# Kernel optimization log

Measured on AMD Instinct MI355X. Metric: run time of the kernel, lower is better.

The kernel has to match this reference:

```python
import jax, jax.numpy as jnp
import numpy as np

DIM = 1024
HEADS = 16
HEAD_DIM = DIM // HEADS
K_NEIGH = 64  # local_window, adaptive_window=False
SCALE = 1.0 / np.sqrt(HEAD_DIM)


def setup_inputs() -> dict:
    key = jax.random.key(0)
    ks = jax.random.split(key, 6)
    b, n = 1, 4096
    x = jax.random.normal(ks[0], (b, n, DIM), dtype=jnp.float32)
    cantor_coords = jax.random.uniform(ks[1], (n,), dtype=jnp.float32)
    # torch nn.Linear(dim, 3*dim): weight [3*dim, dim]; we store transposed [dim, 3*dim]
    W_qkv = jax.random.normal(ks[2], (DIM, 3 * DIM), dtype=jnp.float32) * (1.0 / np.sqrt(DIM))
    b_qkv = jax.random.normal(ks[3], (3 * DIM,), dtype=jnp.float32) * 0.01
    W_out = jax.random.normal(ks[4], (DIM, DIM), dtype=jnp.float32) * (1.0 / np.sqrt(DIM))
    b_out = jax.random.normal(ks[5], (DIM,), dtype=jnp.float32) * 0.01
    return {"x": x, "cantor_coords": cantor_coords, "W_qkv": W_qkv,
            "b_qkv": b_qkv, "W_out": W_out, "b_out": b_out}


def _routes(cantor_coords):
    # [n, n] pairwise |c_i - c_j|; k smallest -> top_k of negated distances
    d = jnp.abs(cantor_coords[:, None] - cantor_coords[None, :])
    _, idx = jax.lax.top_k(-d, K_NEIGH)  # [n, k]
    return idx


def reference(x, cantor_coords, W_qkv, b_qkv, W_out, b_out):
    b, n, _ = x.shape
    qkv = x @ W_qkv + b_qkv                          # [b, n, 3*dim]
    qkv = qkv.reshape(b, n, 3, HEADS, HEAD_DIM)
    qkv = jnp.transpose(qkv, (2, 0, 3, 1, 4))        # [3, b, h, n, d]
    q, k, v = qkv[0], qkv[1], qkv[2]

    routes = _routes(cantor_coords)                  # [n, k]
    k_g = k[:, :, routes, :]                         # [b, h, n, k, d]
    v_g = v[:, :, routes, :]
    scores = jnp.einsum('bhqd,bhqkd->bhqk', q, k_g) * SCALE
    attn = jax.nn.softmax(scores, axis=-1)           # dropout p=0 (eval)
    out = jnp.einsum('bhqk,bhqkd->bhqd', attn, v_g)  # [b, h, n, d]
    out = jnp.transpose(out, (0, 2, 1, 3)).reshape(b, n, DIM)
    return out @ W_out + b_out
```

## Files before the change

### kernel.cpp

```cpp
#include <hip/hip_runtime.h>
#include <hip/hip_bf16.h>

typedef _Float16 f16x8 __attribute__((ext_vector_type(8)));
typedef float f32x4 __attribute__((ext_vector_type(4)));
typedef unsigned long long u64;

#define NSEQ 4096
#define DIMM 1024
#define NQKV 3072

#define BAR() asm volatile("s_barrier" ::: "memory")

__device__ __forceinline__ f32x4 mfma16(f16x8 a, f16x8 b, f32x4 c) {
  return __builtin_amdgcn_mfma_f32_16x16x32_f16(a, b, c, 0, 0, 0);
}

__device__ __forceinline__ void glds16(const void* g, void* l) {
  __builtin_amdgcn_global_load_lds(
      (const __attribute__((address_space(1))) void*)g,
      (__attribute__((address_space(3))) void*)l, 16, 0, 0);
}

__global__ __launch_bounds__(256) void prep_kernel(
    const float* __restrict__ x, _Float16* __restrict__ xh,
    const float* __restrict__ Wqkv, _Float16* __restrict__ wqkvt,
    const float* __restrict__ Wout, _Float16* __restrict__ woutt,
    const float* __restrict__ cc, int* __restrict__ sorted_idx,
    float* __restrict__ csort, int* __restrict__ ranko) {
  __shared__ __align__(16) char plds[16640];
  const int bid = blockIdx.x, t = threadIdx.x;
  if (bid < 2048) {
    const int i = bid * 256 + t;
    const float4 a = ((const float4*)x)[i * 2];
    const float4 b = ((const float4*)x)[i * 2 + 1];
    f16x8 o = {(_Float16)a.x, (_Float16)a.y, (_Float16)a.z, (_Float16)a.w,
               (_Float16)b.x, (_Float16)b.y, (_Float16)b.z, (_Float16)b.w};
    ((f16x8*)xh)[i] = o;
  } else if (bid < 3072) {
    const bool qkv = bid < 2816;
    const int sub = qkv ? bid - 2048 : bid - 2816;
    const float* W = qkv ? Wqkv : Wout;
    _Float16* Wt = qkv ? wqkvt : woutt;
    const int Nn = qkv ? 3072 : 1024;
    const int k0 = (sub & 15) * 64, n0 = (sub >> 4) * 64;
    float (*tile)[65] = (float(*)[65])plds;
    const int tx = t & 63, ty = t >> 6;
    for (int rr = ty; rr < 64; rr += 4)
      tile[rr][tx] = W[(size_t)(k0 + rr) * Nn + n0 + tx];
    __syncthreads();
#pragma unroll
    for (int it = 0; it < 2; ++it) {
      const int idx = it * 256 + t;
      const int row = idx >> 3, seg = idx & 7;
      f16x8 v;
#pragma unroll
      for (int j = 0; j < 8; ++j) v[j] = (_Float16)tile[seg * 8 + j][row];
      *(f16x8*)&Wt[(size_t)(n0 + row) * 1024 + k0 + seg * 8] = v;
    }
  } else {
    float* sc = (float*)plds;
#pragma unroll
    for (int it = 0; it < 4; ++it) {
      const int i = it * 256 + t;
      ((float4*)sc)[i] = ((const float4*)cc)[i];
    }
    __syncthreads();
    const int elem = (bid - 3072) * 32 + (t >> 3);
    const int s = t & 7;
    const unsigned mybits = __float_as_uint(sc[elem]);
    int cnt = 0;
#pragma unroll 8
    for (int m = 0; m < 512; ++m) {
      const int j = s + (m << 3);
      const unsigned bj = __float_as_uint(sc[j]);
      cnt += (bj < mybits || (bj == mybits && j < elem)) ? 1 : 0;
    }
    cnt += __shfl_xor(cnt, 1);
    cnt += __shfl_xor(cnt, 2);
    cnt += __shfl_xor(cnt, 4);
    if (s == 0) {
      sorted_idx[cnt] = elem;
      csort[cnt] = sc[elem];
      ranko[elem] = cnt;
    }
  }
}

__global__ __launch_bounds__(512) void mask_kernel(
    const float* __restrict__ csort, const int* __restrict__ sorted_idx,
    unsigned* __restrict__ masks) {
  const int tid = threadIdx.x, lane = tid & 63, wid = tid >> 6;
  const int p = blockIdx.x * 8 + wid;
  int W0 = 64 * (p >> 6) - 64;
  W0 = min(max(W0, 0), NSEQ - 192);
  const float cp = csort[p];
  u64 key[4];
#pragma unroll
  for (int r = 0; r < 3; ++r) {
    const int w = r * 64 + lane;
    const float d = fabsf(csort[W0 + w] - cp);
    key[r] = (((u64)__float_as_uint(d)) << 20) |
             (((u64)(unsigned)sorted_idx[W0 + w]) << 8) | (unsigned)w;
  }
  key[3] = ~0ull;
#pragma unroll
  for (int k = 2; k <= 256; k <<= 1) {
#pragma unroll
    for (int j = k >> 1; j > 0; j >>= 1) {
      if (j >= 64) {
        const int rj = j >> 6;
#pragma unroll
        for (int r = 0; r < 4; ++r) {
          const int rp = r ^ rj;
          if (rp > r) {
            const bool up = (((r * 64) & k) == 0);
            const u64 a = key[r], b2 = key[rp];
            const bool sw = (a > b2) == up;
            key[r] = sw ? b2 : a;
            key[rp] = sw ? a : b2;
          }
        }
      } else {
#pragma unroll
        for (int r = 0; r < 4; ++r) {
          const u64 pv = __shfl_xor(key[r], j);
          const bool up = (((r * 64 + lane) & k) == 0);
          const bool lower = ((lane & j) == 0);
          const bool takemin = (lower == up);
          const u64 mn = key[r] < pv ? key[r] : pv;
          const u64 mx = key[r] < pv ? pv : key[r];
          key[r] = takemin ? mn : mx;
        }
      }
    }
  }
  const unsigned w0 = (unsigned)(key[0] & 0xffu);
  const unsigned hi = w0 >> 5, bit = 1u << (w0 & 31u);
  unsigned m0w = hi == 0 ? bit : 0u;
  unsigned m1w = hi == 1 ? bit : 0u;
  unsigned m2w = hi == 2 ? bit : 0u;
  unsigned m3w = hi == 3 ? bit : 0u;
  unsigned m4w = hi == 4 ? bit : 0u;
  unsigned m5w = hi == 5 ? bit : 0u;
#pragma unroll
  for (int s = 1; s < 64; s <<= 1) {
    m0w |= __shfl_xor(m0w, s);
    m1w |= __shfl_xor(m1w, s);
    m2w |= __shfl_xor(m2w, s);
    m3w |= __shfl_xor(m3w, s);
    m4w |= __shfl_xor(m4w, s);
    m5w |= __shfl_xor(m5w, s);
  }
  if (lane < 8) {
    unsigned val = 0u;
    val = lane == 0 ? m0w : val;
    val = lane == 1 ? m1w : val;
    val = lane == 2 ? m2w : val;
    val = lane == 3 ? m3w : val;
    val = lane == 4 ? m4w : val;
    val = lane == 5 ? m5w : val;
    masks[p * 8 + lane] = val;
  }
}

__device__ __forceinline__ f16x8 ldsfrag(const char* base, int r, int g) {
  return *(const f16x8*)(base + r * 128 + ((g ^ (r & 7)) << 4));
}

__device__ __forceinline__ void stage_half(const char* gbase, size_t kb, int t,
                                           char* lds_half, int tid) {
#pragma unroll
  for (int s = 0; s < 2; ++s) {
    const int rel = tid * 16 + s * 8192;
    const int r = rel >> 7;
    const int g = (rel >> 4) & 7;
    const int gg = g ^ (r & 7);
    glds16(gbase + (size_t)r * kb + t * 128 + gg * 16, lds_half + rel);
  }
}

__device__ __forceinline__ void stage_64r(const char* gbase, size_t kb, int t,
                                          char* lds8k, int tid) {
  const int rel = tid * 16;
  const int r = rel >> 7;
  const int g = (rel >> 4) & 7;
  const int gg = g ^ (r & 7);
  glds16(gbase + (size_t)r * kb + t * 128 + gg * 16, lds8k + rel);
}

__device__ __forceinline__ void rd_b3(const char* Bb, int wn, int lr, int kg,
                                      f16x8 (&bf)[3][2]) {
#pragma unroll
  for (int nt = 0; nt < 3; ++nt) {
    bf[nt][0] = ldsfrag(Bb, wn + nt * 16 + lr, kg);
    bf[nt][1] = ldsfrag(Bb, wn + nt * 16 + lr, 4 + kg);
  }
}

template <int Q>
__device__ __forceinline__ void rd_a(const char* Ab, int wm, int lr, int kg,
                                     f16x8 (&af)[2][2]) {
#pragma unroll
  for (int m = 0; m < 2; ++m) {
    af[m][0] = ldsfrag(Ab, wm + (2 * Q + m) * 16 + lr, kg);
    af[m][1] = ldsfrag(Ab, wm + (2 * Q + m) * 16 + lr, 4 + kg);
  }
}

template <int Q>
__device__ __forceinline__ void do_mfma3(const f16x8 (&af)[2][2],
                                         const f16x8 (&bf)[3][2],
                                         f32x4 (&acc)[8][3]) {
#pragma unroll
  for (int m = 0; m < 2; ++m)
#pragma unroll
    for (int nt = 0; nt < 3; ++nt) {
      acc[2 * Q + m][nt] = mfma16(af[m][0], bf[nt][0], acc[2 * Q + m][nt]);
      acc[2 * Q + m][nt] = mfma16(af[m][1], bf[nt][1], acc[2 * Q + m][nt]);
    }
}

template <bool LAST>
__device__ __forceinline__ void ktile_pair192(const char* Ag, const char* Bg,
                                              size_t kb, char* smem, int tid,
                                              int wm, int wn, int lr, int kg,
                                              int t1, int t2, int t3,
                                              f32x4 (&acc)[8][3]) {
  char* A0 = smem;
  char* A1 = smem + 32768;
  char* B0 = smem + 65536;
  char* B1 = smem + 65536 + 24576;
  f16x8 bf[3][2], af[2][2];
  rd_b3(B0, wn, lr, kg, bf);
  rd_a<0>(A0, wm, lr, kg, af);
  stage_64r(Ag, kb, t1, A1, tid);
  stage_64r(Ag + 64 * kb, kb, t1, A1 + 8192, tid);
  BAR();
  __builtin_amdgcn_s_setprio(1);
  do_mfma3<0>(af, bf, acc);
  __builtin_amdgcn_s_setprio(0);
  BAR();
  rd_a<1>(A0, wm, lr, kg, af);
  stage_64r(Ag + 128 * kb, kb, t1, A1 + 16384, tid);
  stage_64r(Ag + 192 * kb, kb, t1, A1 + 24576, tid);
  BAR();
  __builtin_amdgcn_s_setprio(1);
  do_mfma3<1>(af, bf, acc);
  __builtin_amdgcn_s_setprio(0);
  BAR();
  rd_a<2>(A0, wm, lr, kg, af);
  if (!LAST) {
    stage_64r(Bg, kb, t2, B0, tid);
    stage_64r(Bg + 64 * kb, kb, t2, B0 + 8192, tid);
  }
  BAR();
  __builtin_amdgcn_s_setprio(1);
  do_mfma3<2>(af, bf, acc);
  __builtin_amdgcn_s_setprio(0);
  BAR();
  rd_a<3>(A0, wm, lr, kg, af);
  if (!LAST) stage_64r(Bg + 128 * kb, kb, t2, B0 + 16384, tid);
  BAR();
  __builtin_amdgcn_s_setprio(1);
  do_mfma3<3>(af, bf, acc);
  __builtin_amdgcn_s_setprio(0);
  if (LAST)
    asm volatile("s_waitcnt vmcnt(0)" ::: "memory");
  else
    asm volatile("s_waitcnt vmcnt(3)" ::: "memory");
  BAR();
  rd_b3(B1, wn, lr, kg, bf);
  rd_a<0>(A1, wm, lr, kg, af);
  if (!LAST) {
    stage_64r(Ag, kb, t2, A0, tid);
    stage_64r(Ag + 64 * kb, kb, t2, A0 + 8192, tid);
  }
  BAR();
  __builtin_amdgcn_s_setprio(1);
  do_mfma3<0>(af, bf, acc);
  __builtin_amdgcn_s_setprio(0);
  BAR();
  rd_a<1>(A1, wm, lr, kg, af);
  if (!LAST) {
    stage_64r(Ag + 128 * kb, kb, t2, A0 + 16384, tid);
    stage_64r(Ag + 192 * kb, kb, t2, A0 + 24576, tid);
  }
  BAR();
  __builtin_amdgcn_s_setprio(1);
  do_mfma3<1>(af, bf, acc);
  __builtin_amdgcn_s_setprio(0);
  BAR();
  rd_a<2>(A1, wm, lr, kg, af);
  if (!LAST) {
    stage_64r(Bg, kb, t3, B1, tid);
    stage_64r(Bg + 64 * kb, kb, t3, B1 + 8192, tid);
  }
  BAR();
  __builtin_amdgcn_s_setprio(1);
  do_mfma3<2>(af, bf, acc);
  __builtin_amdgcn_s_setprio(0);
  BAR();
  rd_a<3>(A1, wm, lr, kg, af);
  if (!LAST) stage_64r(Bg + 128 * kb, kb, t3, B1 + 16384, tid);
  BAR();
  __builtin_amdgcn_s_setprio(1);
  do_mfma3<3>(af, bf, acc);
  __builtin_amdgcn_s_setprio(0);
  if (!LAST) asm volatile("s_waitcnt vmcnt(3)" ::: "memory");
  BAR();
}

__global__ __launch_bounds__(512, 2) void qkv_gemm192_kernel(
    const _Float16* __restrict__ A, const _Float16* __restrict__ Bt,
    const float* __restrict__ bias, const int* __restrict__ ranko,
    _Float16* __restrict__ C) {
  extern __shared__ char smem[];
  const int NN = 3072;
  const size_t kb = 2048;
  const int tid = threadIdx.x;
  const int lane = tid & 63, wid = tid >> 6;
  const int lr = lane & 15, kg = lane >> 4;
  const int wm = (wid >> 2) * 128, wn = (wid & 3) * 48;
  const int r8 = blockIdx.x & 7, idx = blockIdx.x >> 3;
  const int bx = (r8 & 3) * 4 + (idx >> 3);
  const int by = (r8 >> 2) * 8 + (idx & 7);
  const int m0 = bx * 256, n0 = by * 192;
  const char* Ag = (const char*)A + (size_t)m0 * kb;
  const char* Bg = (const char*)Bt + (size_t)n0 * kb;
  char* A0 = smem;
  char* B0 = smem + 65536;
  char* B1 = smem + 65536 + 24576;
  f32x4 acc[8][3] = {};
#pragma unroll
  for (int u = 0; u < 4; ++u)
    stage_64r(Ag + (size_t)(64 * u) * kb, kb, 0, A0 + u * 8192, tid);
#pragma unroll
  for (int u = 0; u < 3; ++u)
    stage_64r(Bg + (size_t)(64 * u) * kb, kb, 0, B0 + u * 8192, tid);
#pragma unroll
  for (int u = 0; u < 3; ++u)
    stage_64r(Bg + (size_t)(64 * u) * kb, kb, 1, B1 + u * 8192, tid);
  asm volatile("s_waitcnt vmcnt(3)" ::: "memory");
  BAR();
#pragma unroll 1
  for (int i = 0; i < 7; ++i)
    ktile_pair192<false>(Ag, Bg, kb, smem, tid, wm, wn, lr, kg, 2 * i + 1,
                         2 * i + 2, 2 * i + 3, acc);
  ktile_pair192<true>(Ag, Bg, kb, smem, tid, wm, wn, lr, kg, 15, 16, 17, acc);
#pragma unroll
  for (int mt = 0; mt < 8; ++mt) {
    const int row0 = m0 + wm + mt * 16 + kg * 4;
    int srow[4];
#pragma unroll
    for (int rr = 0; rr < 4; ++rr) srow[rr] = ranko[row0 + rr];
#pragma unroll
    for (int nt = 0; nt < 3; ++nt) {
      const int col = n0 + wn + nt * 16 + lr;
      const float bv = bias[col];
#pragma unroll
      for (int rr = 0; rr < 4; ++rr)
        C[(size_t)srow[rr] * NN + col] = (_Float16)(acc[mt][nt][rr] + bv);
    }
  }
}

__global__ __launch_bounds__(512, 2) void out_gemm128_kernel(
    const _Float16* __restrict__ A, const _Float16* __restrict__ Bt,
    const float* __restrict__ bias, float* __restrict__ C) {
  extern __shared__ char smem[];
  const size_t kb = 2048;
  const int tid = threadIdx.x;
  const int lane = tid & 63, wid = tid >> 6;
  const int lr = lane & 15, kg = lane >> 4;
  const int wm = (wid >> 2) * 64, wn = (wid & 3) * 32;
  const int r8 = blockIdx.x & 7, idx = blockIdx.x >> 3;
  const int bx = (r8 & 3) * 8 + (idx >> 2);
  const int by = (r8 >> 2) * 4 + (idx & 3);
  const int m0 = bx * 128, n0 = by * 128;
  const char* Ag = (const char*)A + (size_t)m0 * kb;
  const char* Bg = (const char*)Bt + (size_t)n0 * kb;
  f32x4 acc[4][2] = {};
  stage_half(Ag, kb, 0, smem, tid);
  stage_half(Bg, kb, 0, smem + 49152, tid);
  stage_half(Ag, kb, 1, smem + 16384, tid);
  stage_half(Bg, kb, 1, smem + 49152 + 16384, tid);
  asm volatile("s_waitcnt vmcnt(4)" ::: "memory");
  BAR();
#pragma unroll
  for (int t = 0; t < 16; ++t) {
    const char* At = smem + (t % 3) * 16384;
    const char* Bb = smem + 49152 + (t % 3) * 16384;
    f16x8 bf[2][2], af[4][2];
#pragma unroll
    for (int nt = 0; nt < 2; ++nt) {
      bf[nt][0] = ldsfrag(Bb, wn + nt * 16 + lr, kg);
      bf[nt][1] = ldsfrag(Bb, wn + nt * 16 + lr, 4 + kg);
    }
#pragma unroll
    for (int m = 0; m < 4; ++m) {
      af[m][0] = ldsfrag(At, wm + m * 16 + lr, kg);
      af[m][1] = ldsfrag(At, wm + m * 16 + lr, 4 + kg);
    }
    if (t < 14) {
      stage_half(Ag, kb, t + 2, smem + ((t + 2) % 3) * 16384, tid);
      stage_half(Bg, kb, t + 2, smem + 49152 + ((t + 2) % 3) * 16384, tid);
    }
    BAR();
    __builtin_amdgcn_s_setprio(1);
#pragma unroll
    for (int m = 0; m < 4; ++m)
#pragma unroll
      for (int nt = 0; nt < 2; ++nt) {
        acc[m][nt] = mfma16(af[m][0], bf[nt][0], acc[m][nt]);
        acc[m][nt] = mfma16(af[m][1], bf[nt][1], acc[m][nt]);
      }
    __builtin_amdgcn_s_setprio(0);
    if (t < 14)
      asm volatile("s_waitcnt vmcnt(4)" ::: "memory");
    else if (t == 14)
      asm volatile("s_waitcnt vmcnt(0)" ::: "memory");
    BAR();
  }
#pragma unroll
  for (int nt = 0; nt < 2; ++nt) {
    const int col = n0 + wn + nt * 16 + lr;
    const float bv = bias[col];
#pragma unroll
    for (int mt = 0; mt < 4; ++mt) {
      const int row0 = m0 + wm + mt * 16 + kg * 4;
#pragma unroll
      for (int rr = 0; rr < 4; ++rr)
        C[(size_t)(row0 + rr) * 1024 + col] = acc[mt][nt][rr] + bv;
    }
  }
}

__global__ __launch_bounds__(256) void attn_kernel(
    const _Float16* __restrict__ qkvs, const unsigned* __restrict__ masks,
    const int* __restrict__ sorted_idx, _Float16* __restrict__ attn_h) {
  __shared__ __align__(128) char sK[24576];
  __shared__ __align__(128) char sV[24576];
  const int flat = (blockIdx.x & 7) * 128 + (blockIdx.x >> 3);
  const int b = flat & 63, h = flat >> 6;
  const int tid = threadIdx.x, lane = tid & 63, wid = tid >> 6;
  const int W0 = min(max(64 * b - 64, 0), NSEQ - 192);
  const int lrow16 = lane & 15, kgrp = lane >> 4;
#pragma unroll
  for (int c = 0; c < 6; ++c) {
    const int o = c * 4096 + wid * 1024 + lane * 16;
    const int row = o >> 7;
    const int inrow = (o & 127) ^ ((row & 7) << 4);
    glds16((const char*)qkvs + (size_t)(W0 + row) * 6144 + 2048 + h * 128 + inrow,
           sK + o);
  }
  f16x8 vreg[6];
#pragma unroll
  for (int c = 0; c < 6; ++c) {
    const int o = c * 4096 + wid * 1024 + lane * 16;
    vreg[c] = *(const f16x8*)((const char*)qkvs + (size_t)(W0 + (o >> 7)) * 6144 +
                              4096 + h * 128 + (o & 127));
  }
  const int p_base = b * 64 + wid * 16;
  const char* qp =
      (const char*)qkvs + (size_t)(p_base + lrow16) * 6144 + h * 128 + kgrp * 16;
  const f16x8 aq0 = *(const f16x8*)qp;
  const f16x8 aq1 = *(const f16x8*)(qp + 64);
  unsigned mb[4];
#pragma unroll
  for (int r = 0; r < 4; ++r) {
    const int p = p_base + kgrp * 4 + r;
    const uint4 wa = *(const uint4*)&masks[p * 8];
    const uint2 wb2 = *(const uint2*)&masks[p * 8 + 4];
    const unsigned wsv6[6] = {wa.x, wa.y, wa.z, wa.w, wb2.x, wb2.y};
    unsigned bits = 0;
#pragma unroll
    for (int n = 0; n < 12; ++n)
      bits |= ((wsv6[n >> 1] >> (((n & 1) << 4) + lrow16)) & 1u) << n;
    mb[r] = bits;
  }
  const int lrot = lane & 7;
#pragma unroll
  for (int c = 0; c < 6; ++c) {
    const int o = c * 4096 + wid * 1024 + lane * 16;
    const int k = o >> 7;
    const int d0 = (o & 127) >> 1;
#pragma unroll
    for (int ee = 0; ee < 8; ++ee) {
      const int e = (ee + lrot) & 7;
      const int d = d0 + e;
      *(_Float16*)(sV + d * 384 + ((2 * k) ^ ((d & 7) << 4))) = vreg[c][e];
    }
  }
  __syncthreads();
  float sv[12][4];
#pragma unroll
  for (int n = 0; n < 12; ++n) {
    const int j = n * 16 + lrow16;
    const int sw = (j & 7) << 4;
    const char* kr = sK + j * 128;
    const f16x8 b0 = *(const f16x8*)(kr + ((kgrp * 16) ^ sw));
    const f16x8 b1 = *(const f16x8*)(kr + ((64 + kgrp * 16) ^ sw));
    f32x4 a = {};
    a = mfma16(aq0, b0, a);
    a = mfma16(aq1, b1, a);
#pragma unroll
    for (int r = 0; r < 4; ++r)
      sv[n][r] = ((mb[r] >> n) & 1u) ? a[r] * 0.125f : -1e30f;
  }
#pragma unroll
  for (int r = 0; r < 4; ++r) {
    float m = sv[0][r];
#pragma unroll
    for (int n = 1; n < 12; ++n) m = fmaxf(m, sv[n][r]);
    m = fmaxf(m, __shfl_xor(m, 1));
    m = fmaxf(m, __shfl_xor(m, 2));
    m = fmaxf(m, __shfl_xor(m, 4));
    m = fmaxf(m, __shfl_xor(m, 8));
    float s = 0.f;
#pragma unroll
    for (int n = 0; n < 12; ++n) {
      const float e = __expf(sv[n][r] - m);
      sv[n][r] = e;
      s += e;
    }
    s += __shfl_xor(s, 1);
    s += __shfl_xor(s, 2);
    s += __shfl_xor(s, 4);
    s += __shfl_xor(s, 8);
    const float rinv = 1.f / s;
#pragma unroll
    for (int n = 0; n < 12; ++n) sv[n][r] *= rinv;
  }
  __syncthreads();
#pragma unroll
  for (int n = 0; n < 12; ++n) {
#pragma unroll
    for (int r = 0; r < 4; ++r) {
      const int lrw = wid * 16 + kgrp * 4 + r;
      const int cb = (n * 16 + lrow16) * 2;
      *(_Float16*)(sK + lrw * 384 + (cb ^ ((lrw & 7) << 4))) = (_Float16)sv[n][r];
    }
  }
  __syncthreads();
  f32x4 oacc[4] = {};
  const int arow = wid * 16 + lrow16;
  const int swa = (arow & 7) << 4;
#pragma unroll
  for (int kt = 0; kt < 6; ++kt) {
    const int kbo = kt * 64 + kgrp * 16;
    const f16x8 pa = *(const f16x8*)(sK + arow * 384 + (kbo ^ swa));
#pragma unroll
    for (int nt = 0; nt < 4; ++nt) {
      const int d = nt * 16 + lrow16;
      const f16x8 vb = *(const f16x8*)(sV + d * 384 + (kbo ^ ((d & 7) << 4)));
      oacc[nt] = mfma16(pa, vb, oacc[nt]);
    }
  }
#pragma unroll
  for (int r = 0; r < 4; ++r) {
    const int p = p_base + kgrp * 4 + r;
    const int orig = sorted_idx[p];
    _Float16* op = attn_h + (size_t)orig * DIMM + h * 64;
#pragma unroll
    for (int nt = 0; nt < 4; ++nt)
      op[nt * 16 + lrow16] = (_Float16)oacc[nt][r];
  }
}

extern "C" void kernel_launch(void* const* d_in, const int* in_sizes, int n_in,
                              void* d_out, int out_size, void* d_ws, size_t ws_size,
                              hipStream_t stream) {
  const float* x = (const float*)d_in[0];
  const float* cc = (const float*)d_in[1];
  const float* Wqkv = (const float*)d_in[2];
  const float* bqkv = (const float*)d_in[3];
  const float* Wout = (const float*)d_in[4];
  const float* bout = (const float*)d_in[5];
  char* ws = (char*)d_ws;

  _Float16* xh = (_Float16*)(ws + 0);
  _Float16* wqkvt = (_Float16*)(ws + 8388608);
  _Float16* woutt = (_Float16*)(ws + 14680064);
  _Float16* qkvs = (_Float16*)(ws + 16777216);
  _Float16* atnh = (_Float16*)(ws + 41943040);
  int* sidx = (int*)(ws + 50331648);
  float* csort = (float*)(ws + 50348032);
  int* rankb = (int*)(ws + 50364416);
  unsigned* msk = (unsigned*)(ws + 50380800);

  hipFuncSetAttribute((const void*)qkv_gemm192_kernel,
                      hipFuncAttributeMaxDynamicSharedMemorySize, 114688);
  hipFuncSetAttribute((const void*)out_gemm128_kernel,
                      hipFuncAttributeMaxDynamicSharedMemorySize, 98304);

  prep_kernel<<<3200, 256, 0, stream>>>(x, xh, Wqkv, wqkvt, Wout, woutt, cc,
                                        sidx, csort, rankb);
  mask_kernel<<<512, 512, 0, stream>>>(csort, sidx, msk);
  qkv_gemm192_kernel<<<256, 512, 114688, stream>>>(xh, wqkvt, bqkv, rankb,
                                                   qkvs);
  attn_kernel<<<1024, 256, 0, stream>>>(qkvs, msk, sidx, atnh);
  out_gemm128_kernel<<<256, 512, 98304, stream>>>(atnh, woutt, bout,
                                                  (float*)d_out);
}
```

Measured before the change: 102.8 us.

## Shrink QKV GEMM tile from 256x192 to 128x192 with more blocks

Retiles the QKV projection GEMM so each block computes 128 rows instead of 256. The grid doubles to 512 blocks, LDS drops to 80 KB, and launch bounds now allow more resident blocks. The k-tile pipeline is restructured to match: fewer MFMA phases per tile, and the B-tile staging and waitcnt counts are rescheduled. The aim is better occupancy and CU balance on the 256-CU device, at the cost of lower data reuse per block and more global traffic for B.

```diff
diff --git a/kernel.cpp b/kernel.cpp
--- a/kernel.cpp
+++ b/kernel.cpp
@@ -208,9 +208,9 @@
 }
 
 template <int Q>
-__device__ __forceinline__ void do_mfma3(const f16x8 (&af)[2][2],
+__device__ __forceinline__ void do_mfma2(const f16x8 (&af)[2][2],
                                          const f16x8 (&bf)[3][2],
-                                         f32x4 (&acc)[8][3]) {
+                                         f32x4 (&acc)[4][3]) {
 #pragma unroll
   for (int m = 0; m < 2; ++m)
 #pragma unroll
@@ -221,96 +221,64 @@
 }
 
 template <bool LAST>
-__device__ __forceinline__ void ktile_pair192(const char* Ag, const char* Bg,
+__device__ __forceinline__ void ktile_pair128(const char* Ag, const char* Bg,
                                               size_t kb, char* smem, int tid,
                                               int wm, int wn, int lr, int kg,
                                               int t1, int t2, int t3,
-                                              f32x4 (&acc)[8][3]) {
+                                              f32x4 (&acc)[4][3]) {
   char* A0 = smem;
-  char* A1 = smem + 32768;
-  char* B0 = smem + 65536;
-  char* B1 = smem + 65536 + 24576;
+  char* A1 = smem + 16384;
+  char* B0 = smem + 32768;
+  char* B1 = smem + 57344;
   f16x8 bf[3][2], af[2][2];
   rd_b3(B0, wn, lr, kg, bf);
   rd_a<0>(A0, wm, lr, kg, af);
-  stage_64r(Ag, kb, t1, A1, tid);
-  stage_64r(Ag + 64 * kb, kb, t1, A1 + 8192, tid);
+  stage_half(Ag, kb, t1, A1, tid);
   BAR();
   __builtin_amdgcn_s_setprio(1);
-  do_mfma3<0>(af, bf, acc);
+  do_mfma2<0>(af, bf, acc);
   __builtin_amdgcn_s_setprio(0);
   BAR();
   rd_a<1>(A0, wm, lr, kg, af);
-  stage_64r(Ag + 128 * kb, kb, t1, A1 + 16384, tid);
-  stage_64r(Ag + 192 * kb, kb, t1, A1 + 24576, tid);
-  BAR();
-  __builtin_amdgcn_s_setprio(1);
-  do_mfma3<1>(af, bf, acc);
-  __builtin_amdgcn_s_setprio(0);
-  BAR();
-  rd_a<2>(A0, wm, lr, kg, af);
   if (!LAST) {
     stage_64r(Bg, kb, t2, B0, tid);
     stage_64r(Bg + 64 * kb, kb, t2, B0 + 8192, tid);
   }
   BAR();
   __builtin_amdgcn_s_setprio(1);
-  do_mfma3<2>(af, bf, acc);
-  __builtin_amdgcn_s_setprio(0);
-  BAR();
-  rd_a<3>(A0, wm, lr, kg, af);
-  if (!LAST) stage_64r(Bg + 128 * kb, kb, t2, B0 + 16384, tid);
-  BAR();
-  __builtin_amdgcn_s_setprio(1);
-  do_mfma3<3>(af, bf, acc);
+  do_mfma2<1>(af, bf, acc);
   __builtin_amdgcn_s_setprio(0);
   if (LAST)
     asm volatile("s_waitcnt vmcnt(0)" ::: "memory");
   else
-    asm volatile("s_waitcnt vmcnt(3)" ::: "memory");
+    asm volatile("s_waitcnt vmcnt(2)" ::: "memory");
   BAR();
   rd_b3(B1, wn, lr, kg, bf);
   rd_a<0>(A1, wm, lr, kg, af);
   if (!LAST) {
-    stage_64r(Ag, kb, t2, A0, tid);
-    stage_64r(Ag + 64 * kb, kb, t2, A0 + 8192, tid);
+    stage_64r(Bg + 128 * kb, kb, t2, B0 + 16384, tid);
+    stage_half(Ag, kb, t2, A0, tid);
   }
   BAR();
   __builtin_amdgcn_s_setprio(1);
-  do_mfma3<0>(af, bf, acc);
+  do_mfma2<0>(af, bf, acc);
   __builtin_amdgcn_s_setprio(0);
   BAR();
   rd_a<1>(A1, wm, lr, kg, af);
-  if (!LAST) {
-    stage_64r(Ag + 128 * kb, kb, t2, A0 + 16384, tid);
-    stage_64r(Ag + 192 * kb, kb, t2, A0 + 24576, tid);
-  }
-  BAR();
-  __builtin_amdgcn_s_setprio(1);
-  do_mfma3<1>(af, bf, acc);
-  __builtin_amdgcn_s_setprio(0);
-  BAR();
-  rd_a<2>(A1, wm, lr, kg, af);
   if (!LAST) {
     stage_64r(Bg, kb, t3, B1, tid);
     stage_64r(Bg + 64 * kb, kb, t3, B1 + 8192, tid);
+    stage_64r(Bg + 128 * kb, kb, t3, B1 + 16384, tid);
   }
   BAR();
   __builtin_amdgcn_s_setprio(1);
-  do_mfma3<2>(af, bf, acc);
-  __builtin_amdgcn_s_setprio(0);
-  BAR();
-  rd_a<3>(A1, wm, lr, kg, af);
-  if (!LAST) stage_64r(Bg + 128 * kb, kb, t3, B1 + 16384, tid);
-  BAR();
-  __builtin_amdgcn_s_setprio(1);
-  do_mfma3<3>(af, bf, acc);
+  do_mfma2<1>(af, bf, acc);
   __builtin_amdgcn_s_setprio(0);
   if (!LAST) asm volatile("s_waitcnt vmcnt(3)" ::: "memory");
   BAR();
 }
 
-__global__ __launch_bounds__(512, 2) void qkv_gemm192_kernel(
+__global__ __launch_bounds__(512, 4) void qkv_gemm128_kernel(
     const _Float16* __restrict__ A, const _Float16* __restrict__ Bt,
     const float* __restrict__ bias, const int* __restrict__ ranko,
     _Float16* __restrict__ C) {
@@ -320,20 +288,18 @@
   const int tid = threadIdx.x;
   const int lane = tid & 63, wid = tid >> 6;
   const int lr = lane & 15, kg = lane >> 4;
-  const int wm = (wid >> 2) * 128, wn = (wid & 3) * 48;
+  const int wm = (wid >> 2) * 64, wn = (wid & 3) * 48;
   const int r8 = blockIdx.x & 7, idx = blockIdx.x >> 3;
-  const int bx = (r8 & 3) * 4 + (idx >> 3);
+  const int bx = (r8 & 3) * 8 + (idx >> 3);
   const int by = (r8 >> 2) * 8 + (idx & 7);
-  const int m0 = bx * 256, n0 = by * 192;
+  const int m0 = bx * 128, n0 = by * 192;
   const char* Ag = (const char*)A + (size_t)m0 * kb;
   const char* Bg = (const char*)Bt + (size_t)n0 * kb;
   char* A0 = smem;
-  char* B0 = smem + 65536;
-  char* B1 = smem + 65536 + 24576;
-  f32x4 acc[8][3] = {};
-#pragma unroll
-  for (int u = 0; u < 4; ++u)
-    stage_64r(Ag + (size_t)(64 * u) * kb, kb, 0, A0 + u * 8192, tid);
+  char* B0 = smem + 32768;
+  char* B1 = smem + 57344;
+  f32x4 acc[4][3] = {};
+  stage_half(Ag, kb, 0, A0, tid);
 #pragma unroll
   for (int u = 0; u < 3; ++u)
     stage_64r(Bg + (size_t)(64 * u) * kb, kb, 0, B0 + u * 8192, tid);
@@ -344,11 +310,11 @@
   BAR();
 #pragma unroll 1
   for (int i = 0; i < 7; ++i)
-    ktile_pair192<false>(Ag, Bg, kb, smem, tid, wm, wn, lr, kg, 2 * i + 1,
+    ktile_pair128<false>(Ag, Bg, kb, smem, tid, wm, wn, lr, kg, 2 * i + 1,
                          2 * i + 2, 2 * i + 3, acc);
-  ktile_pair192<true>(Ag, Bg, kb, smem, tid, wm, wn, lr, kg, 15, 16, 17, acc);
-#pragma unroll
-  for (int mt = 0; mt < 8; ++mt) {
+  ktile_pair128<true>(Ag, Bg, kb, smem, tid, wm, wn, lr, kg, 15, 16, 17, acc);
+#pragma unroll
+  for (int mt = 0; mt < 4; ++mt) {
     const int row0 = m0 + wm + mt * 16 + kg * 4;
     int srow[4];
 #pragma unroll
@@ -588,16 +554,16 @@
   int* rankb = (int*)(ws + 50364416);
   unsigned* msk = (unsigned*)(ws + 50380800);
 
-  hipFuncSetAttribute((const void*)qkv_gemm192_kernel,
-                      hipFuncAttributeMaxDynamicSharedMemorySize, 114688);
+  hipFuncSetAttribute((const void*)qkv_gemm128_kernel,
+                      hipFuncAttributeMaxDynamicSharedMemorySize, 81920);
   hipFuncSetAttribute((const void*)out_gemm128_kernel,
                       hipFuncAttributeMaxDynamicSharedMemorySize, 98304);
 
   prep_kernel<<<3200, 256, 0, stream>>>(x, xh, Wqkv, wqkvt, Wout, woutt, cc,
                                         sidx, csort, rankb);
   mask_kernel<<<512, 512, 0, stream>>>(csort, sidx, msk);
-  qkv_gemm192_kernel<<<256, 512, 114688, stream>>>(xh, wqkvt, bqkv, rankb,
-                                                   qkvs);
+  qkv_gemm128_kernel<<<512, 512, 81920, stream>>>(xh, wqkvt, bqkv, rankb,
+                                                  qkvs);
   attn_kernel<<<1024, 256, 0, stream>>>(qkvs, msk, sidx, atnh);
   out_gemm128_kernel<<<256, 512, 98304, stream>>>(atnh, woutt, bout,
                                                   (float*)d_out);
```

Result: slower. 105.6 us (+2.7%).
